# Optimization experiments

Measured on AMD Instinct MI355X. Metric: run time of the kernel, lower is better.

The kernel has to match this reference:

```python
import jax, jax.numpy as jnp
import numpy as np

B, C, H, W = 1, 256, 96, 96   # inplanes=256
P = 64                        # planes=64


def setup_inputs() -> dict:
    key = jax.random.key(0)
    ks = jax.random.split(key, 8)
    x = jax.random.normal(ks[0], (B, C, H, W), dtype=jnp.float32)
    y = jax.random.normal(ks[1], (B, C, H, W), dtype=jnp.float32)
    # 1x1 convs == channel matmuls; torch init: normal(0, 0.01), zero bias
    Wv = 0.01 * jax.random.normal(ks[2], (C, C), dtype=jnp.float32)  # conv_value (no bias)
    Wq = 0.01 * jax.random.normal(ks[3], (P, C), dtype=jnp.float32)
    bq = jnp.zeros((P,), dtype=jnp.float32)
    Wk = 0.01 * jax.random.normal(ks[4], (P, C), dtype=jnp.float32)
    bk = jnp.zeros((P,), dtype=jnp.float32)
    # gamma initializes to 0 in the module; use 0.5 so the output is nontrivial
    gamma = jnp.full((1,), 0.5, dtype=jnp.float32)
    return {"x": x, "y": y, "Wv": Wv, "Wq": Wq, "bq": bq, "Wk": Wk, "bk": bk, "gamma": gamma}


def reference(x, y, Wv, Wq, bq, Wk, bk, gamma):
    b, c, h, w = x.shape
    n = h * w                       # query positions (from x)
    m = y.shape[2] * y.shape[3]     # key/value positions (from y)
    xf = x.reshape(b, c, n)         # [B, C, N]
    yf = y.reshape(b, c, m)         # [B, C, M]

    value = jnp.einsum('oc,bcm->bom', Wv, yf)                    # [B, C, M]
    query = jnp.einsum('pc,bcn->bpn', Wq, xf) + bq[None, :, None]  # [B, P, N]
    key_ = jnp.einsum('pc,bcm->bpm', Wk, yf) + bk[None, :, None]   # [B, P, M]

    # mean-centering over spatial dim
    query = query - query.mean(axis=2, keepdims=True)
    key_ = key_ - key_.mean(axis=2, keepdims=True)

    sim = jnp.einsum('bpn,bpm->bnm', query, key_)   # [B, N, M]
    sim = jax.nn.softmax(sim, axis=2)
    out = jnp.einsum('bnm,bcm->bcn', sim, value)    # [B, C, N]
    out = out.reshape(b, c, h, w)
    return gamma[0] * out
```

## Files before the change

### kernel.cpp

```cpp
#include <hip/hip_runtime.h>


typedef __attribute__((ext_vector_type(8))) short short8;
typedef __attribute__((ext_vector_type(8))) unsigned short ushort8;
typedef __attribute__((ext_vector_type(4))) float f32x4;

#define C_DIM 256
#define P_DIM 64
#define N_DIM 9216
#define NT    144
#define SPLITS 4
#define MQ    (N_DIM / SPLITS)
#define KV_TILES (MQ / 64)

__device__ __forceinline__ unsigned short f2b(float f) {
  unsigned int u = __float_as_uint(f);
  u += 0x7fffu + ((u >> 16) & 1u);
  return (unsigned short)(u >> 16);
}

__device__ __forceinline__ float b2f(unsigned short h) {
  return __uint_as_float(((unsigned int)h) << 16);
}

__device__ __forceinline__ f32x4 mfma16(short8 a, short8 b, f32x4 c) {
  return __builtin_amdgcn_mfma_f32_16x16x32_bf16(a, b, c, 0, 0, 0);
}

__global__ void k1_mean_conv(const float* __restrict__ x, const float* __restrict__ y,
                             unsigned short* __restrict__ xb, unsigned short* __restrict__ yb,
                             float* __restrict__ xmean, float* __restrict__ ymean) {
  int b = blockIdx.x;
  const float* src = (b < C_DIM) ? x : y;
  unsigned short* dst = (b < C_DIM) ? xb : yb;
  float* mout = (b < C_DIM) ? xmean : ymean;
  int c = b & (C_DIM - 1);
  const float4* row = (const float4*)(src + (size_t)c * N_DIM);
  ushort4* orow = (ushort4*)(dst + (size_t)c * N_DIM);
  int tid = threadIdx.x;
  float s = 0.f;
  for (int i = tid; i < N_DIM / 4; i += 256) {
    float4 v = row[i];
    s += v.x + v.y + v.z + v.w;
    ushort4 o;
    o.x = f2b(v.x); o.y = f2b(v.y); o.z = f2b(v.z); o.w = f2b(v.w);
    orow[i] = o;
  }
#pragma unroll
  for (int off = 1; off < 64; off <<= 1) s += __shfl_xor(s, off);
  __shared__ float red[4];
  if ((tid & 63) == 0) red[tid >> 6] = s;
  __syncthreads();
  if (tid == 0) mout[c] = (red[0] + red[1] + red[2] + red[3]) * (1.f / (float)N_DIM);
}

__global__ void k2_wconv(const float* __restrict__ Wv, const float* __restrict__ Wq,
                         const float* __restrict__ Wk,
                         const float* __restrict__ xmean, const float* __restrict__ ymean,
                         unsigned short* __restrict__ Wvb, unsigned short* __restrict__ Wqb,
                         unsigned short* __restrict__ Wkb,
                         float* __restrict__ qmean, float* __restrict__ kmean) {
  int b = blockIdx.x, t = threadIdx.x;
  if (b < 256) {
    int i = b * 256 + t; Wvb[i] = f2b(Wv[i]);
  } else if (b < 320) {
    int i = (b - 256) * 256 + t; Wqb[i] = f2b(Wq[i]);
  } else if (b < 384) {
    int i = (b - 320) * 256 + t; Wkb[i] = f2b(Wk[i]);
  } else if (t < 128) {
    int p = t & 63;
    const float* W = (t < 64) ? Wq : Wk;
    const float* mv = (t < 64) ? xmean : ymean;
    float s = 0.f;
    for (int cc = 0; cc < 256; cc++) s += W[p * 256 + cc] * mv[cc];
    ((t < 64) ? qmean : kmean)[p] = s;
  }
}

__global__ void k3_proj(const unsigned short* __restrict__ xb, const unsigned short* __restrict__ yb,
                        const unsigned short* __restrict__ Wvb, const unsigned short* __restrict__ Wqb,
                        const unsigned short* __restrict__ Wkb,
                        const float* __restrict__ qmean, const float* __restrict__ kmean,
                        unsigned short* __restrict__ Qb, unsigned short* __restrict__ Kb,
                        unsigned short* __restrict__ Vb) {
  __shared__ unsigned short T[64][264];
  int b = blockIdx.x;
  int role = b / NT;
  int tile = b % NT;
  int m0 = tile * 64;
  int tid = threadIdx.x;
  int w = tid >> 6, lane = tid & 63, l16 = lane & 15, g4 = lane >> 4;

  const unsigned short* src = (role == 1) ? xb : yb;
  {
    int c = tid;
    const unsigned short* sr = src + (size_t)c * N_DIM + m0;
#pragma unroll
    for (int j = 0; j < 8; j++) {
      ushort8 v = *(const ushort8*)&sr[j * 8];
#pragma unroll
      for (int i = 0; i < 8; i++) T[j * 8 + i][c] = v[i];
    }
  }
  __syncthreads();

  if (role == 0) {
    f32x4 acc[4][4];
#pragma unroll
    for (int rf = 0; rf < 4; rf++)
#pragma unroll
      for (int cf = 0; cf < 4; cf++) acc[rf][cf] = (f32x4)0.f;
#pragma unroll
    for (int kk = 0; kk < 8; kk++) {
      short8 bf[4];
#pragma unroll
      for (int cf = 0; cf < 4; cf++)
        bf[cf] = *(const short8*)&T[cf * 16 + l16][kk * 32 + g4 * 8];
#pragma unroll
      for (int rf = 0; rf < 4; rf++) {
        short8 af = *(const short8*)&Wvb[(size_t)(w * 64 + rf * 16 + l16) * 256 + kk * 32 + g4 * 8];
#pragma unroll
        for (int cf = 0; cf < 4; cf++) acc[rf][cf] = mfma16(af, bf[cf], acc[rf][cf]);
      }
    }
#pragma unroll
    for (int rf = 0; rf < 4; rf++)
#pragma unroll
      for (int cf = 0; cf < 4; cf++)
#pragma unroll
        for (int r = 0; r < 4; r++) {
          int co = w * 64 + rf * 16 + g4 * 4 + r;
          int m = m0 + cf * 16 + l16;
          Vb[(size_t)co * N_DIM + m] = f2b(acc[rf][cf][r]);
        }
  } else {
    const unsigned short* Wb = (role == 1) ? Wqb : Wkb;
    const float* mean = (role == 1) ? qmean : kmean;
    unsigned short* Ob = (role == 1) ? Qb : Kb;
    f32x4 acc[4];
#pragma unroll
    for (int cf = 0; cf < 4; cf++) acc[cf] = (f32x4)0.f;
#pragma unroll
    for (int kk = 0; kk < 8; kk++) {
      short8 af = *(const short8*)&T[w * 16 + l16][kk * 32 + g4 * 8];
#pragma unroll
      for (int cf = 0; cf < 4; cf++) {
        short8 bf = *(const short8*)&Wb[(size_t)(cf * 16 + l16) * 256 + kk * 32 + g4 * 8];
        acc[cf] = mfma16(af, bf, acc[cf]);
      }
    }
#pragma unroll
    for (int cf = 0; cf < 4; cf++)
#pragma unroll
      for (int r = 0; r < 4; r++) {
        int n = m0 + w * 16 + g4 * 4 + r;
        int p = cf * 16 + l16;
        Ob[(size_t)n * 64 + p] = f2b(acc[cf][r] - mean[p]);
      }
  }
}

__global__ __launch_bounds__(256, 3)
void k4_attn(const unsigned short* __restrict__ Qb, const unsigned short* __restrict__ Kb,
             const unsigned short* __restrict__ Vb,
             unsigned short* __restrict__ po, float* __restrict__ m_arr, float* __restrict__ l_arr) {
  __shared__ unsigned short Vt[256][72];
  __shared__ unsigned short Pt[64][72];

  int b = blockIdx.x;
  int s = b & (SPLITS - 1);
  int n0 = (b >> 2) * 64;
  int tid = threadIdx.x;
  int w = tid >> 6, lane = tid & 63, l16 = lane & 15, g4 = lane >> 4;

  short8 qf[2];
  {
    const unsigned short* qrow = Qb + (size_t)(n0 + w * 16 + l16) * 64;
    qf[0] = *(const short8*)&qrow[g4 * 8];
    qf[1] = *(const short8*)&qrow[32 + g4 * 8];
  }

  f32x4 acc[16];
#pragma unroll
  for (int i = 0; i < 16; i++) acc[i] = (f32x4)0.f;
  float mreg[4], lreg[4];
#pragma unroll
  for (int r = 0; r < 4; r++) { mreg[r] = -3e38f; lreg[r] = 0.f; }

  int mbase = s * MQ;

  ushort8 vreg[8];
  {
    const ushort8* vsrc = (const ushort8*)(Vb + (size_t)tid * N_DIM + mbase);
#pragma unroll
    for (int j = 0; j < 8; j++) vreg[j] = vsrc[j];
  }

  for (int t = 0; t < KV_TILES; t++) {
    int m0 = mbase + t * 64;
    if (t) __syncthreads();
#pragma unroll
    for (int j = 0; j < 8; j++) *(ushort8*)&Vt[tid][j * 8] = vreg[j];
    __syncthreads();

    f32x4 sa[4];
#pragma unroll
    for (int cf = 0; cf < 4; cf++) sa[cf] = (f32x4)0.f;
#pragma unroll
    for (int kk = 0; kk < 2; kk++) {
#pragma unroll
      for (int cf = 0; cf < 4; cf++) {
        short8 kf = *(const short8*)&Kb[(size_t)(m0 + cf * 16 + l16) * 64 + kk * 32 + g4 * 8];
        sa[cf] = mfma16(qf[kk], kf, sa[cf]);
      }
    }

    if (t + 1 < KV_TILES) {
      const ushort8* vsrc = (const ushort8*)(Vb + (size_t)tid * N_DIM + m0 + 64);
#pragma unroll
      for (int j = 0; j < 8; j++) vreg[j] = vsrc[j];
    }

    float f[4];
#pragma unroll
    for (int r = 0; r < 4; r++) {
      float v = fmaxf(fmaxf(sa[0][r], sa[1][r]), fmaxf(sa[2][r], sa[3][r]));
#pragma unroll
      for (int off = 1; off < 16; off <<= 1) v = fmaxf(v, __shfl_xor(v, off));
      float mnew = fmaxf(mreg[r], v);
      f[r] = __expf(mreg[r] - mnew);
      mreg[r] = mnew;
    }
#pragma unroll
    for (int cf = 0; cf < 4; cf++)
#pragma unroll
      for (int r = 0; r < 4; r++) sa[cf][r] = __expf(sa[cf][r] - mreg[r]);
#pragma unroll
    for (int r = 0; r < 4; r++) {
      float sv = sa[0][r] + sa[1][r] + sa[2][r] + sa[3][r];
#pragma unroll
      for (int off = 1; off < 16; off <<= 1) sv += __shfl_xor(sv, off);
      lreg[r] = lreg[r] * f[r] + sv;
    }
#pragma unroll
    for (int cfc = 0; cfc < 16; cfc++)
#pragma unroll
      for (int r = 0; r < 4; r++) acc[cfc][r] *= f[r];

#pragma unroll
    for (int cf = 0; cf < 4; cf++)
#pragma unroll
      for (int r = 0; r < 4; r++)
        Pt[w * 16 + g4 * 4 + r][cf * 16 + l16] = f2b(sa[cf][r]);

#pragma unroll
    for (int kk = 0; kk < 2; kk++) {
      short8 pf = *(const short8*)&Pt[w * 16 + l16][kk * 32 + g4 * 8];
#pragma unroll
      for (int cfc = 0; cfc < 16; cfc++) {
        short8 vf = *(const short8*)&Vt[cfc * 16 + l16][kk * 32 + g4 * 8];
        acc[cfc] = mfma16(pf, vf, acc[cfc]);
      }
    }
  }

  unsigned short* poS = po + (size_t)s * N_DIM * C_DIM;
#pragma unroll
  for (int cfc = 0; cfc < 16; cfc++)
#pragma unroll
    for (int r = 0; r < 4; r++) {
      int n = n0 + w * 16 + g4 * 4 + r;
      int c = cfc * 16 + l16;
      poS[(size_t)n * C_DIM + c] = f2b(acc[cfc][r]);
    }
  if (l16 == 0) {
#pragma unroll
    for (int r = 0; r < 4; r++) {
      int n = n0 + w * 16 + g4 * 4 + r;
      m_arr[s * N_DIM + n] = mreg[r];
      l_arr[s * N_DIM + n] = lreg[r];
    }
  }
}

__global__ void k5_combine(const unsigned short* __restrict__ po, const float* __restrict__ m_arr,
                           const float* __restrict__ l_arr, const float* __restrict__ gamma,
                           float* __restrict__ out) {
  __shared__ float TT[64][65];
  int b = blockIdx.x;
  int c0 = (b & 3) * 64;
  int n0 = (b >> 2) * 64;
  float g = gamma[0];
  int tid = threadIdx.x;
#pragma unroll
  for (int rr = 0; rr < 16; rr++) {
    int idx = rr * 256 + tid;
    int nl = idx >> 6, cl = idx & 63;
    int n = n0 + nl;
    float m0v = m_arr[n], m1v = m_arr[N_DIM + n];
    float m2v = m_arr[2 * N_DIM + n], m3v = m_arr[3 * N_DIM + n];
    float M = fmaxf(fmaxf(m0v, m1v), fmaxf(m2v, m3v));
    float w0 = __expf(m0v - M), w1 = __expf(m1v - M);
    float w2 = __expf(m2v - M), w3 = __expf(m3v - M);
    float denom = l_arr[n] * w0 + l_arr[N_DIM + n] * w1 +
                  l_arr[2 * N_DIM + n] * w2 + l_arr[3 * N_DIM + n] * w3;
    float v0 = b2f(po[(size_t)n * C_DIM + c0 + cl]);
    float v1 = b2f(po[((size_t)N_DIM + n) * C_DIM + c0 + cl]);
    float v2 = b2f(po[((size_t)2 * N_DIM + n) * C_DIM + c0 + cl]);
    float v3 = b2f(po[((size_t)3 * N_DIM + n) * C_DIM + c0 + cl]);
    TT[cl][nl] = (v0 * w0 + v1 * w1 + v2 * w2 + v3 * w3) / denom;
  }
  __syncthreads();
#pragma unroll
  for (int rr = 0; rr < 16; rr++) {
    int idx = rr * 256 + tid;
    int cl = idx >> 6, nl = idx & 63;
    out[(size_t)(c0 + cl) * N_DIM + n0 + nl] = g * TT[cl][nl];
  }
}

extern "C" void kernel_launch(void* const* d_in, const int* in_sizes, int n_in,
                              void* d_out, int out_size, void* d_ws, size_t ws_size,
                              hipStream_t stream) {
  const float* x  = (const float*)d_in[0];
  const float* y  = (const float*)d_in[1];
  const float* Wv = (const float*)d_in[2];
  const float* Wq = (const float*)d_in[3];
  const float* Wk = (const float*)d_in[5];
  const float* gamma = (const float*)d_in[7];
  float* out = (float*)d_out;

  char* ws = (char*)d_ws;
  constexpr size_t OFF_XMEAN = 0;
  constexpr size_t OFF_YMEAN = 1024;
  constexpr size_t OFF_QMEAN = 2048;
  constexpr size_t OFF_KMEAN = 2560;
  constexpr size_t OFF_XB    = 4096;
  constexpr size_t OFF_YB    = OFF_XB + 4718592;
  constexpr size_t OFF_WVB   = OFF_YB + 4718592;
  constexpr size_t OFF_WQB   = OFF_WVB + 131072;
  constexpr size_t OFF_WKB   = OFF_WQB + 32768;
  constexpr size_t OFF_QB    = OFF_WKB + 32768;
  constexpr size_t OFF_KB    = OFF_QB + 1179648;
  constexpr size_t OFF_VB    = OFF_KB + 1179648;
  constexpr size_t OFF_PO    = OFF_VB + 4718592;
  constexpr size_t OFF_M     = OFF_PO + (size_t)SPLITS * N_DIM * C_DIM * 2;
  constexpr size_t OFF_L     = OFF_M + (size_t)SPLITS * N_DIM * 4;

  float* xmean = (float*)(ws + OFF_XMEAN);
  float* ymean = (float*)(ws + OFF_YMEAN);
  float* qmean = (float*)(ws + OFF_QMEAN);
  float* kmean = (float*)(ws + OFF_KMEAN);
  unsigned short* xb  = (unsigned short*)(ws + OFF_XB);
  unsigned short* yb  = (unsigned short*)(ws + OFF_YB);
  unsigned short* Wvb = (unsigned short*)(ws + OFF_WVB);
  unsigned short* Wqb = (unsigned short*)(ws + OFF_WQB);
  unsigned short* Wkb = (unsigned short*)(ws + OFF_WKB);
  unsigned short* Qb  = (unsigned short*)(ws + OFF_QB);
  unsigned short* Kb  = (unsigned short*)(ws + OFF_KB);
  unsigned short* Vb  = (unsigned short*)(ws + OFF_VB);
  unsigned short* po  = (unsigned short*)(ws + OFF_PO);
  float* m_arr = (float*)(ws + OFF_M);
  float* l_arr = (float*)(ws + OFF_L);

  k1_mean_conv<<<512, 256, 0, stream>>>(x, y, xb, yb, xmean, ymean);
  k2_wconv<<<385, 256, 0, stream>>>(Wv, Wq, Wk, xmean, ymean, Wvb, Wqb, Wkb, qmean, kmean);
  k3_proj<<<432, 256, 0, stream>>>(xb, yb, Wvb, Wqb, Wkb, qmean, kmean, Qb, Kb, Vb);
  k4_attn<<<NT * SPLITS, 256, 0, stream>>>(Qb, Kb, Vb, po, m_arr, l_arr);
  k5_combine<<<576, 256, 0, stream>>>(po, m_arr, l_arr, gamma, out);
}
```

Baseline: 405.4 us.

## Use single-wave attention blocks reading V fragments directly from global memory

The attention kernel changes from 4-wave blocks that stage V tiles through shared memory with barriers to 1-wave blocks of 16 queries. Each wave loads its V fragments straight from global memory (L2/L1) and raises wave priority around the MFMA sections. This removes the block barriers and the shared-memory staging of V, and adds many more blocks. The cost is that V reuse across waves is lost, so global/cache traffic for V roughly quadruples and V loads are no longer prefetched.

```diff
diff --git a/kernel.cpp b/kernel.cpp
--- a/kernel.cpp
+++ b/kernel.cpp
@@ -160,22 +160,21 @@
   }
 }
 
-__global__ __launch_bounds__(256, 3)
+__global__ __launch_bounds__(64, 3)
 void k4_attn(const unsigned short* __restrict__ Qb, const unsigned short* __restrict__ Kb,
              const unsigned short* __restrict__ Vb,
              unsigned short* __restrict__ po, float* __restrict__ m_arr, float* __restrict__ l_arr) {
-  __shared__ unsigned short Vt[256][72];
-  __shared__ unsigned short Pt[64][72];
+  __shared__ unsigned short Pt[16][72];
 
   int b = blockIdx.x;
   int s = b & (SPLITS - 1);
-  int n0 = (b >> 2) * 64;
-  int tid = threadIdx.x;
-  int w = tid >> 6, lane = tid & 63, l16 = lane & 15, g4 = lane >> 4;
+  int n0 = (b >> 2) * 16;
+  int lane = threadIdx.x;
+  int l16 = lane & 15, g4 = lane >> 4;
 
   short8 qf[2];
   {
-    const unsigned short* qrow = Qb + (size_t)(n0 + w * 16 + l16) * 64;
+    const unsigned short* qrow = Qb + (size_t)(n0 + l16) * 64;
     qf[0] = *(const short8*)&qrow[g4 * 8];
     qf[1] = *(const short8*)&qrow[32 + g4 * 8];
   }
@@ -189,23 +188,13 @@
 
   int mbase = s * MQ;
 
-  ushort8 vreg[8];
-  {
-    const ushort8* vsrc = (const ushort8*)(Vb + (size_t)tid * N_DIM + mbase);
-#pragma unroll
-    for (int j = 0; j < 8; j++) vreg[j] = vsrc[j];
-  }
-
   for (int t = 0; t < KV_TILES; t++) {
     int m0 = mbase + t * 64;
-    if (t) __syncthreads();
-#pragma unroll
-    for (int j = 0; j < 8; j++) *(ushort8*)&Vt[tid][j * 8] = vreg[j];
-    __syncthreads();
 
     f32x4 sa[4];
 #pragma unroll
     for (int cf = 0; cf < 4; cf++) sa[cf] = (f32x4)0.f;
+    __builtin_amdgcn_s_setprio(1);
 #pragma unroll
     for (int kk = 0; kk < 2; kk++) {
 #pragma unroll
@@ -214,12 +203,7 @@
         sa[cf] = mfma16(qf[kk], kf, sa[cf]);
       }
     }
-
-    if (t + 1 < KV_TILES) {
-      const ushort8* vsrc = (const ushort8*)(Vb + (size_t)tid * N_DIM + m0 + 64);
-#pragma unroll
-      for (int j = 0; j < 8; j++) vreg[j] = vsrc[j];
-    }
+    __builtin_amdgcn_s_setprio(0);
 
     float f[4];
 #pragma unroll
@@ -251,17 +235,19 @@
     for (int cf = 0; cf < 4; cf++)
 #pragma unroll
       for (int r = 0; r < 4; r++)
-        Pt[w * 16 + g4 * 4 + r][cf * 16 + l16] = f2b(sa[cf][r]);
-
+        Pt[g4 * 4 + r][cf * 16 + l16] = f2b(sa[cf][r]);
+
+    __builtin_amdgcn_s_setprio(1);
 #pragma unroll
     for (int kk = 0; kk < 2; kk++) {
-      short8 pf = *(const short8*)&Pt[w * 16 + l16][kk * 32 + g4 * 8];
+      short8 pf = *(const short8*)&Pt[l16][kk * 32 + g4 * 8];
 #pragma unroll
       for (int cfc = 0; cfc < 16; cfc++) {
-        short8 vf = *(const short8*)&Vt[cfc * 16 + l16][kk * 32 + g4 * 8];
+        short8 vf = *(const short8*)&Vb[(size_t)(cfc * 16 + l16) * N_DIM + m0 + kk * 32 + g4 * 8];
         acc[cfc] = mfma16(pf, vf, acc[cfc]);
       }
     }
+    __builtin_amdgcn_s_setprio(0);
   }
 
   unsigned short* poS = po + (size_t)s * N_DIM * C_DIM;
@@ -269,14 +255,14 @@
   for (int cfc = 0; cfc < 16; cfc++)
 #pragma unroll
     for (int r = 0; r < 4; r++) {
-      int n = n0 + w * 16 + g4 * 4 + r;
+      int n = n0 + g4 * 4 + r;
       int c = cfc * 16 + l16;
       poS[(size_t)n * C_DIM + c] = f2b(acc[cfc][r]);
     }
   if (l16 == 0) {
 #pragma unroll
     for (int r = 0; r < 4; r++) {
-      int n = n0 + w * 16 + g4 * 4 + r;
+      int n = n0 + g4 * 4 + r;
       m_arr[s * N_DIM + n] = mreg[r];
       l_arr[s * N_DIM + n] = lreg[r];
     }
@@ -366,6 +352,6 @@
   k1_mean_conv<<<512, 256, 0, stream>>>(x, y, xb, yb, xmean, ymean);
   k2_wconv<<<385, 256, 0, stream>>>(Wv, Wq, Wk, xmean, ymean, Wvb, Wqb, Wkb, qmean, kmean);
   k3_proj<<<432, 256, 0, stream>>>(xb, yb, Wvb, Wqb, Wkb, qmean, kmean, Qb, Kb, Vb);
-  k4_attn<<<NT * SPLITS, 256, 0, stream>>>(Qb, Kb, Vb, po, m_arr, l_arr);
+  k4_attn<<<(N_DIM / 16) * SPLITS, 64, 0, stream>>>(Qb, Kb, Vb, po, m_arr, l_arr);
   k5_combine<<<576, 256, 0, stream>>>(po, m_arr, l_arr, gamma, out);
 }
```

Result: slower. 498.5 us (+23.0%).
